# Optimization experiments

Measured on AMD Instinct MI355X. Metric: run time of the kernel, lower is better.

Reference implementation:

```python
import jax, jax.numpy as jnp
import numpy as np

D = 256; NH = 8; HD = 32; DFF = 1024; NL = 4; NPT = 4
SHAPES = [(100, 100), (50, 50), (25, 25), (13, 13)]
LEN_V = sum(h * w for h, w in SHAPES)  # 13294
BS = 16; LQ = 300


def _ln(x, g, b):
    m = jnp.mean(x, -1, keepdims=True)
    v = jnp.var(x, -1, keepdims=True)
    return (x - m) * jax.lax.rsqrt(v + 1e-5) * g + b


def _bilinear(v, loc, H, W):
    # v: [bs, nh, H*W, hd]; loc: [bs, Lq, nh, P, 2] normalized [0,1]
    # matches F.grid_sample(bilinear, align_corners=False, padding_mode='zeros')
    bs, Lq, nh, P, _ = loc.shape
    x = loc[..., 0] * W - 0.5
    y = loc[..., 1] * H - 0.5
    x0 = jnp.floor(x); y0 = jnp.floor(y)
    dx = x - x0; dy = y - y0
    x0 = x0.astype(jnp.int32); y0 = y0.astype(jnp.int32)
    out = jnp.zeros((bs, Lq, nh, P, v.shape[-1]), v.dtype)
    for ix, iy, w in ((x0, y0, (1 - dx) * (1 - dy)),
                      (x0 + 1, y0, dx * (1 - dy)),
                      (x0, y0 + 1, (1 - dx) * dy),
                      (x0 + 1, y0 + 1, dx * dy)):
        valid = (ix >= 0) & (ix < W) & (iy >= 0) & (iy < H)
        idx = jnp.clip(iy, 0, H - 1) * W + jnp.clip(ix, 0, W - 1)  # [bs,Lq,nh,P]
        idx = jnp.transpose(idx, (0, 2, 1, 3)).reshape(bs, nh, Lq * P, 1)
        g = jnp.take_along_axis(v, idx, axis=2).reshape(bs, nh, Lq, P, -1)
        g = jnp.transpose(g, (0, 2, 1, 3, 4))  # [bs,Lq,nh,P,hd]
        out = out + g * jnp.where(valid, w, jnp.zeros_like(w))[..., None]
    return out


def reference(tgt, reference_points, memory, Wq, bq, Wk, bk, Wv, bv, Wo, bo,
              Wvp, bvp, Wso, bso, Waw, baw, Wop, bop, W1, bf1, W2, bf2,
              ln1_g, ln1_b, ln2_g, ln2_b, ln3_g, ln3_b):
    bs, Lq, _ = tgt.shape
    # ---- self attention (query_pos_embed=None, attn_mask=None) ----
    qh = (tgt @ Wq + bq).reshape(bs, Lq, NH, HD)
    kh = (tgt @ Wk + bk).reshape(bs, Lq, NH, HD)
    vh = (tgt @ Wv + bv).reshape(bs, Lq, NH, HD)
    scores = jnp.einsum('bqhd,bkhd->bhqk', qh, kh) * np.float32(1.0 / np.sqrt(HD))
    attn = jax.nn.softmax(scores, -1)
    sa = jnp.einsum('bhqk,bkhd->bqhd', attn, vh).reshape(bs, Lq, D) @ Wo + bo
    t = _ln(tgt + sa, ln1_g, ln1_b)
    # ---- PP multi-scale deformable cross attention ----
    val = (memory @ Wvp + bvp).reshape(bs, LEN_V, NH, HD)
    val = jnp.transpose(val, (0, 2, 1, 3))  # [bs, nh, Lv, hd]
    off = (t @ Wso + bso).reshape(bs, Lq, NH, NL, NPT, 2)
    aw = jax.nn.softmax((t @ Waw + baw).reshape(bs, Lq, NH, NL * NPT), -1)
    aw = aw.reshape(bs, Lq, NH, NL, NPT)
    rp = reference_points  # [bs, Lq, NL, 4] -> (cx, cy, w, h) branch
    loc = rp[:, :, None, :, None, :2] + off / NPT * rp[:, :, None, :, None, 2:] * 0.5
    start = 0
    ca = jnp.zeros((bs, Lq, NH, HD), t.dtype)
    for l, (H, W) in enumerate(SHAPES):
        v_l = val[:, :, start:start + H * W]
        sampled = _bilinear(v_l, loc[:, :, :, l], H, W)  # [bs,Lq,nh,P,hd]
        ca = ca + jnp.einsum('bqhpd,bqhp->bqhd', sampled, aw[:, :, :, l])
        start += H * W
    ca = ca.reshape(bs, Lq, D) @ Wop + bop
    t = _ln(t + ca, ln2_g, ln2_b)
    # ---- FFN ----
    ff = jax.nn.relu(t @ W1 + bf1) @ W2 + bf2
    return _ln(t + ff, ln3_g, ln3_b)


def setup_inputs() -> dict:
    ks = iter(jax.random.split(jax.random.key(0), 64))
    inp = {}
    inp['tgt'] = jax.random.normal(next(ks), (BS, LQ, D), jnp.float32)
    inp['reference_points'] = jax.random.uniform(next(ks), (BS, LQ, NL, 4), jnp.float32)
    inp['memory'] = jax.random.normal(next(ks), (BS, LEN_V, D), jnp.float32)
    for name, sh in [('Wq', (D, D)), ('Wk', (D, D)), ('Wv', (D, D)), ('Wo', (D, D)),
                     ('Wvp', (D, D)), ('Wso', (D, NH * NL * NPT * 2)),
                     ('Waw', (D, NH * NL * NPT)), ('Wop', (D, D)),
                     ('W1', (D, DFF)), ('W2', (DFF, D))]:
        inp[name] = jax.random.normal(next(ks), sh, jnp.float32) * 0.02
    for name, dim in [('bq', D), ('bk', D), ('bv', D), ('bo', D), ('bvp', D),
                      ('bso', NH * NL * NPT * 2), ('baw', NH * NL * NPT),
                      ('bop', D), ('bf1', DFF), ('bf2', D)]:
        inp[name] = jnp.zeros((dim,), jnp.float32)
    for g, b in [('ln1_g', 'ln1_b'), ('ln2_g', 'ln2_b'), ('ln3_g', 'ln3_b')]:
        inp[g] = jnp.ones((D,), jnp.float32)
        inp[b] = jnp.zeros((D,), jnp.float32)
    return inp
```

## Files before the change

kernel.cpp:

```cpp
#include <hip/hip_runtime.h>
#include <hip/hip_bf16.h>
#include <cstddef>

#define D_    256
#define NH_   8
#define HD_   32
#define LQ_   300
#define BS_   16
#define LENV_ 13294
#define DFF_  1024
#define NROWS (BS_*LQ_)
#define VROWS (BS_*LENV_)

typedef __attribute__((ext_vector_type(8))) short short8;
typedef __attribute__((ext_vector_type(4))) float f32x4;
typedef unsigned int u32;

__device__ __forceinline__ short f2bf(float x) {
    unsigned u = __float_as_uint(x);
    u += 0x7fff + ((u >> 16) & 1);
    return (short)(u >> 16);
}
__device__ __forceinline__ unsigned pack_bf2(float lo, float hi) {
    return (unsigned)(unsigned short)f2bf(lo) | ((unsigned)(unsigned short)f2bf(hi) << 16);
}
__device__ __forceinline__ float bf2f(short s) {
    return __uint_as_float((unsigned)(unsigned short)s << 16);
}

__global__ __launch_bounds__(256) void prep_all(
    const float* __restrict__ Wq, const float* __restrict__ Wk,
    const float* __restrict__ Wv, const float* __restrict__ Wo,
    const float* __restrict__ Wvp, const float* __restrict__ Wso,
    const float* __restrict__ Waw, const float* __restrict__ Wop,
    const float* __restrict__ W1, const float* __restrict__ W2,
    const float* __restrict__ bqp, const float* __restrict__ bkp,
    const float* __restrict__ bvp, const float* __restrict__ bsop,
    const float* __restrict__ bawp,
    short* __restrict__ Wqkvt, short* __restrict__ Wot,
    short* __restrict__ Wvpt, short* __restrict__ Wsoawt,
    short* __restrict__ Wopt, short* __restrict__ W1t,
    short* __restrict__ W2t, float* __restrict__ bqkv,
    float* __restrict__ bsoaw)
{
    const int blk = blockIdx.x, tid = threadIdx.x;
    if (blk < 1792) {
        const int seg = blk >> 8;
        const int e = ((blk & 255) << 8) | tid;
        const int n = e >> 8, k = e & 255;
        const float* src; short* dst;
        switch (seg) {
            case 0: src = Wq;  dst = Wqkvt;          break;
            case 1: src = Wk;  dst = Wqkvt + 65536;  break;
            case 2: src = Wv;  dst = Wqkvt + 131072; break;
            case 3: src = Wo;  dst = Wot;            break;
            case 4: src = Wvp; dst = Wvpt;           break;
            case 5: src = Wso; dst = Wsoawt;         break;
            default: src = Wop; dst = Wopt;          break;
        }
        dst[e] = f2bf(src[(size_t)k * 256 + n]);
    } else if (blk < 1920) {
        const int e = ((blk - 1792) << 8) | tid;
        const int n = e >> 8, k = e & 255;
        Wsoawt[65536 + e] = f2bf(Waw[(size_t)k * 128 + n]);
    } else if (blk < 2048) {
        const int e = ((blk - 1920) << 8) | tid;
        Wsoawt[98304 + e] = 0;
    } else if (blk < 3072) {
        const int e = ((blk - 2048) << 8) | tid;
        const int n = e >> 8, k = e & 255;
        W1t[e] = f2bf(W1[(size_t)k * 1024 + n]);
    } else if (blk < 4096) {
        const int e = ((blk - 3072) << 8) | tid;
        const int n = e / 1024, k = e % 1024;
        W2t[e] = f2bf(W2[(size_t)k * 256 + n]);
    } else {
        const int e = ((blk - 4096) << 8) | tid;
        if (e < 768)
            bqkv[e] = (e < 256) ? bqp[e] : (e < 512) ? bkp[e - 256] : bvp[e - 512];
        else if (e < 1280) {
            const int f = e - 768;
            bsoaw[f] = (f < 256) ? bsop[f] : (f < 384) ? bawp[f - 256] : 0.f;
        }
    }
}

template<int ACT, int OUT_BF16, int STACKED, int FUSE_LN>
__global__ __launch_bounds__(256) void mfma_gemm(
    const float* __restrict__ A, const short* __restrict__ Wt,
    const float* __restrict__ bias, void* __restrict__ Cout,
    int M, int N, int K,
    const float* __restrict__ resid, const float* __restrict__ lng,
    const float* __restrict__ lnb)
{
    __shared__ short Alds[2][64 * 40];
    __shared__ short Blds[2][256 * 40];
    const int tid  = threadIdx.x;
    const int lane = tid & 63;
    const int wn   = tid >> 6;
    const int m0   = blockIdx.x * 64;
    const int nb   = blockIdx.y;
    const int srow = tid >> 2;
    const int schk = tid & 3;

    const int  arow = m0 + srow;
    const bool aok  = (arow < M);
    const float* aptr = &A[(size_t)(aok ? arow : 0) * K + schk * 8];
    const short* bptr = &Wt[(size_t)(nb * 256 + srow) * K + schk * 8];

    f32x4 acc[4][4] = {};
    float4 ra0, ra1;
    short8 rb0, rb1, rb2, rb3;

    ra0 = make_float4(0.f, 0.f, 0.f, 0.f); ra1 = ra0;
    if (aok) { ra0 = *(const float4*)(aptr); ra1 = *(const float4*)(aptr + 4); }
    rb0 = *(const short8*)(bptr);
    rb1 = *(const short8*)(bptr + (size_t)64 * K);
    rb2 = *(const short8*)(bptr + (size_t)128 * K);
    rb3 = *(const short8*)(bptr + (size_t)192 * K);
    {
        short8 s;
        s[0] = f2bf(ra0.x); s[1] = f2bf(ra0.y); s[2] = f2bf(ra0.z); s[3] = f2bf(ra0.w);
        s[4] = f2bf(ra1.x); s[5] = f2bf(ra1.y); s[6] = f2bf(ra1.z); s[7] = f2bf(ra1.w);
        *(short8*)&Alds[0][srow * 40 + schk * 8] = s;
        *(short8*)&Blds[0][(srow +   0) * 40 + schk * 8] = rb0;
        *(short8*)&Blds[0][(srow +  64) * 40 + schk * 8] = rb1;
        *(short8*)&Blds[0][(srow + 128) * 40 + schk * 8] = rb2;
        *(short8*)&Blds[0][(srow + 192) * 40 + schk * 8] = rb3;
    }
    __syncthreads();

    const int lg = lane >> 4;
    const int lr = lane & 15;
    int buf = 0;

    for (int k0 = 32; k0 < K; k0 += 32) {
        ra0 = make_float4(0.f, 0.f, 0.f, 0.f); ra1 = ra0;
        if (aok) { ra0 = *(const float4*)(aptr + k0); ra1 = *(const float4*)(aptr + k0 + 4); }
        rb0 = *(const short8*)(bptr + k0);
        rb1 = *(const short8*)(bptr + k0 + (size_t)64 * K);
        rb2 = *(const short8*)(bptr + k0 + (size_t)128 * K);
        rb3 = *(const short8*)(bptr + k0 + (size_t)192 * K);

        {
            short8 a[4], b[4];
            #pragma unroll
            for (int mr = 0; mr < 4; ++mr)
                a[mr] = *(const short8*)&Alds[buf][(mr * 16 + lr) * 40 + lg * 8];
            #pragma unroll
            for (int nr = 0; nr < 4; ++nr)
                b[nr] = *(const short8*)&Blds[buf][(wn * 64 + nr * 16 + lr) * 40 + lg * 8];
            #pragma unroll
            for (int mr = 0; mr < 4; ++mr)
                #pragma unroll
                for (int nr = 0; nr < 4; ++nr)
                    acc[mr][nr] = __builtin_amdgcn_mfma_f32_16x16x32_bf16(
                        a[mr], b[nr], acc[mr][nr], 0, 0, 0);
        }

        {
            short8 s;
            s[0] = f2bf(ra0.x); s[1] = f2bf(ra0.y); s[2] = f2bf(ra0.z); s[3] = f2bf(ra0.w);
            s[4] = f2bf(ra1.x); s[5] = f2bf(ra1.y); s[6] = f2bf(ra1.z); s[7] = f2bf(ra1.w);
            const int ob = buf ^ 1;
            *(short8*)&Alds[ob][srow * 40 + schk * 8] = s;
            *(short8*)&Blds[ob][(srow +   0) * 40 + schk * 8] = rb0;
            *(short8*)&Blds[ob][(srow +  64) * 40 + schk * 8] = rb1;
            *(short8*)&Blds[ob][(srow + 128) * 40 + schk * 8] = rb2;
            *(short8*)&Blds[ob][(srow + 192) * 40 + schk * 8] = rb3;
        }
        __syncthreads();
        buf ^= 1;
    }

    {
        short8 a[4], b[4];
        #pragma unroll
        for (int mr = 0; mr < 4; ++mr)
            a[mr] = *(const short8*)&Alds[buf][(mr * 16 + lr) * 40 + lg * 8];
        #pragma unroll
        for (int nr = 0; nr < 4; ++nr)
            b[nr] = *(const short8*)&Blds[buf][(wn * 64 + nr * 16 + lr) * 40 + lg * 8];
        #pragma unroll
        for (int mr = 0; mr < 4; ++mr)
            #pragma unroll
            for (int nr = 0; nr < 4; ++nr)
                acc[mr][nr] = __builtin_amdgcn_mfma_f32_16x16x32_bf16(
                    a[mr], b[nr], acc[mr][nr], 0, 0, 0);
    }

    if (FUSE_LN) {
        __shared__ float RedS[4][64];
        __shared__ float RedS2[4][64];
        float psum[4][4] = {};
        float psq[4][4]  = {};
        #pragma unroll
        for (int mr = 0; mr < 4; ++mr)
            #pragma unroll
            for (int r4 = 0; r4 < 4; ++r4) {
                const int row = m0 + mr * 16 + lg * 4 + r4;
                #pragma unroll
                for (int nr = 0; nr < 4; ++nr) {
                    const int col = wn * 64 + nr * 16 + lr;
                    float x = acc[mr][nr][r4] + bias[col]
                            + resid[(size_t)row * 256 + col];
                    acc[mr][nr][r4] = x;
                    psum[mr][r4] += x;
                    psq[mr][r4]  += x * x;
                }
            }
        #pragma unroll
        for (int o = 1; o < 16; o <<= 1)
            #pragma unroll
            for (int mr = 0; mr < 4; ++mr)
                #pragma unroll
                for (int r4 = 0; r4 < 4; ++r4) {
                    psum[mr][r4] += __shfl_xor(psum[mr][r4], o);
                    psq[mr][r4]  += __shfl_xor(psq[mr][r4], o);
                }
        if (lr == 0) {
            #pragma unroll
            for (int mr = 0; mr < 4; ++mr)
                #pragma unroll
                for (int r4 = 0; r4 < 4; ++r4) {
                    const int lrow = mr * 16 + lg * 4 + r4;
                    RedS[wn][lrow]  = psum[mr][r4];
                    RedS2[wn][lrow] = psq[mr][r4];
                }
        }
        __syncthreads();
        float* outp = (float*)Cout;
        #pragma unroll
        for (int mr = 0; mr < 4; ++mr)
            #pragma unroll
            for (int r4 = 0; r4 < 4; ++r4) {
                const int lrow = mr * 16 + lg * 4 + r4;
                const int row  = m0 + lrow;
                const float s  = RedS[0][lrow] + RedS[1][lrow] + RedS[2][lrow] + RedS[3][lrow];
                const float s2 = RedS2[0][lrow] + RedS2[1][lrow] + RedS2[2][lrow] + RedS2[3][lrow];
                const float mean = s * (1.f / 256.f);
                const float var  = s2 * (1.f / 256.f) - mean * mean;
                const float inv  = rsqrtf(var + 1e-5f);
                #pragma unroll
                for (int nr = 0; nr < 4; ++nr) {
                    const int col = wn * 64 + nr * 16 + lr;
                    outp[(size_t)row * 256 + col] =
                        (acc[mr][nr][r4] - mean) * inv * lng[col] + lnb[col];
                }
            }
        return;
    }

    if (STACKED) {
        float* Cb = (float*)Cout + (size_t)nb * M * 256;
        const float* bb = bias + nb * 256;
        #pragma unroll
        for (int mr = 0; mr < 4; ++mr)
            #pragma unroll
            for (int r = 0; r < 4; ++r) {
                const int row = m0 + mr * 16 + lg * 4 + r;
                if (row >= M) continue;
                #pragma unroll
                for (int nr = 0; nr < 4; ++nr) {
                    const int col = wn * 64 + nr * 16 + lr;
                    Cb[(size_t)row * 256 + col] = acc[mr][nr][r] + bb[col];
                }
            }
    } else {
        #pragma unroll
        for (int mr = 0; mr < 4; ++mr)
            #pragma unroll
            for (int r = 0; r < 4; ++r) {
                const int row = m0 + mr * 16 + lg * 4 + r;
                if (row >= M) continue;
                #pragma unroll
                for (int nr = 0; nr < 4; ++nr) {
                    const int col = nb * 256 + wn * 64 + nr * 16 + lr;
                    float v = acc[mr][nr][r] + bias[col];
                    if (ACT) v = fmaxf(v, 0.f);
                    if (OUT_BF16) ((short*)Cout)[(size_t)row * N + col] = f2bf(v);
                    else          ((float*)Cout)[(size_t)row * N + col] = v;
                }
            }
    }
}

__global__ __launch_bounds__(256, 2) void vp_gemm(
    const float* __restrict__ A, const short* __restrict__ Wt,
    const float* __restrict__ bias, short* __restrict__ C)
{
    __shared__ float Alds[2][32 * 256];
    __shared__ short Cst[32 * 256];
    const int tid  = threadIdx.x;
    const int lane = tid & 63;
    const int w    = tid >> 6;
    const int lr   = lane & 15;
    const int lg   = lane >> 4;

    short8 bf[4][8];
    #pragma unroll
    for (int nr = 0; nr < 4; ++nr) {
        const short* wp = &Wt[(size_t)(w * 64 + nr * 16 + lr) * 256 + lg * 8];
        #pragma unroll
        for (int kc = 0; kc < 8; ++kc)
            bf[nr][kc] = *(const short8*)(wp + kc * 32);
    }
    float bs[4];
    #pragma unroll
    for (int nr = 0; nr < 4; ++nr) bs[nr] = bias[w * 64 + nr * 16 + lr];

    const int NT = VROWS / 32;
    const int NB = 512;

    #define VP_STAGE(BUFI, TILE)                                               \
        {                                                                      \
            _Pragma("unroll")                                                  \
            for (int j = 0; j < 8; ++j) {                                      \
                const int r = w * 8 + j;                                       \
                const int grow = (TILE) * 32 + r;                              \
                const int c16 = ((((lane >> 1) ^ (r & 7)) << 1) | (lane & 1)); \
                const float* src = A + (size_t)grow * 256 + c16 * 4;           \
                __builtin_amdgcn_global_load_lds(                              \
                    (const __attribute__((address_space(1))) u32*)src,         \
                    (__attribute__((address_space(3))) u32*)&Alds[BUFI][r*256],\
                    16, 0, 0);                                                 \
            }                                                                  \
        }

    int t  = blockIdx.x;
    int t2 = t + NB;
    bool has2 = (t2 < NT);
    int buf = 0;

    VP_STAGE(0, t);
    if (has2) VP_STAGE(1, t2);
    if (has2) { asm volatile("s_waitcnt vmcnt(8)" ::: "memory"); }
    else      { asm volatile("s_waitcnt vmcnt(0)" ::: "memory"); }
    __builtin_amdgcn_sched_barrier(0);
    __builtin_amdgcn_s_barrier();

    while (true) {
        f32x4 acc[2][4] = {};
        #pragma unroll
        for (int kc = 0; kc < 8; ++kc) {
            short8 a[2];
            #pragma unroll
            for (int mr = 0; mr < 2; ++mr) {
                const int row = mr * 16 + lr;
                const int c32 = (kc * 4 + lg) ^ (row & 7);
                const float* p = &Alds[buf][row * 256 + c32 * 8];
                float4 x = *(const float4*)(p);
                float4 y = *(const float4*)(p + 4);
                short8 s;
                s[0] = f2bf(x.x); s[1] = f2bf(x.y); s[2] = f2bf(x.z); s[3] = f2bf(x.w);
                s[4] = f2bf(y.x); s[5] = f2bf(y.y); s[6] = f2bf(y.z); s[7] = f2bf(y.w);
                a[mr] = s;
            }
            #pragma unroll
            for (int mr = 0; mr < 2; ++mr)
                #pragma unroll
                for (int nr = 0; nr < 4; ++nr)
                    acc[mr][nr] = __builtin_amdgcn_mfma_f32_16x16x32_bf16(
                        a[mr], bf[nr][kc], acc[mr][nr], 0, 0, 0);
        }

        #pragma unroll
        for (int mr = 0; mr < 2; ++mr)
            #pragma unroll
            for (int r4 = 0; r4 < 4; ++r4)
                #pragma unroll
                for (int nr = 0; nr < 4; ++nr)
                    Cst[(mr * 16 + lg * 4 + r4) * 256 + w * 64 + nr * 16 + lr] =
                        f2bf(acc[mr][nr][r4] + bs[nr]);

        asm volatile("s_waitcnt lgkmcnt(0)" ::: "memory");
        __builtin_amdgcn_sched_barrier(0);
        __builtin_amdgcn_s_barrier();

        const int t3 = t2 + NB;
        const bool has3 = has2 && (t3 < NT);
        if (has3) VP_STAGE(buf, t3);

        {
            const size_t base = (size_t)t * 32 * 256;
            #pragma unroll
            for (int j = 0; j < 4; ++j) {
                const int chunk = j * 256 + tid;
                *(short8*)&C[base + (size_t)chunk * 8] =
                    *(const short8*)&Cst[chunk * 8];
            }
        }

        if (has2) {
            if (has3) { asm volatile("s_waitcnt vmcnt(12)" ::: "memory"); }
            else      { asm volatile("s_waitcnt vmcnt(4)"  ::: "memory"); }
        }
        __builtin_amdgcn_sched_barrier(0);
        __builtin_amdgcn_s_barrier();

        if (!has2) break;
        buf ^= 1;
        t = t2; t2 = t3; has2 = has3;
    }
    #undef VP_STAGE
}

__global__ __launch_bounds__(256) void attn_fused(
    const float* __restrict__ qh, const float* __restrict__ kh,
    const float* __restrict__ vh, float* __restrict__ sa)
{
    __shared__ short Klds[304 * 40];
    __shared__ short Vtlds[32 * 328];
    const int bh = blockIdx.x, b = bh / NH_, h = bh % NH_;
    const int tid = threadIdx.x;

    for (int idx = tid; idx < 304 * 4; idx += 256) {
        const int key = idx >> 2, dc = idx & 3;
        short8 s = {};
        if (key < LQ_) {
            const float* kp = &kh[((size_t)(b * LQ_ + key)) * D_ + h * HD_ + dc * 8];
            float4 a0 = *reinterpret_cast<const float4*>(kp);
            float4 a1 = *reinterpret_cast<const float4*>(kp + 4);
            s[0] = f2bf(a0.x); s[1] = f2bf(a0.y); s[2] = f2bf(a0.z); s[3] = f2bf(a0.w);
            s[4] = f2bf(a1.x); s[5] = f2bf(a1.y); s[6] = f2bf(a1.z); s[7] = f2bf(a1.w);
        }
        *reinterpret_cast<short8*>(&Klds[key * 40 + dc * 8]) = s;
    }
    for (int idx = tid; idx < LQ_ * 8; idx += 256) {
        const int key = idx >> 3, dc = idx & 7;
        const float4 v4 = *reinterpret_cast<const float4*>(
            &vh[((size_t)(b * LQ_ + key)) * D_ + h * HD_ + dc * 4]);
        Vtlds[(dc * 4 + 0) * 328 + key] = f2bf(v4.x);
        Vtlds[(dc * 4 + 1) * 328 + key] = f2bf(v4.y);
        Vtlds[(dc * 4 + 2) * 328 + key] = f2bf(v4.z);
        Vtlds[(dc * 4 + 3) * 328 + key] = f2bf(v4.w);
    }
    for (int idx = tid; idx < 32 * 20; idx += 256) {
        const int d = idx / 20, kk = idx % 20;
        Vtlds[d * 328 + 300 + kk] = 0;
    }
    __syncthreads();

    const int lane = tid & 63;
    const int wid  = tid >> 6;
    const int g    = lane >> 4;
    const int qc   = lane & 15;
    const int y    = blockIdx.y;
    const int qt_end = (y == 0) ? 10 : 19;

    for (int qt = y * 10 + wid; qt < qt_end; qt += 4) {
        const int q0 = qt * 16;
        short8 qf;
        {
            const int q = min(q0 + qc, LQ_ - 1);
            const float* qp = &qh[((size_t)(b * LQ_ + q)) * D_ + h * HD_ + g * 8];
            float4 a0 = *reinterpret_cast<const float4*>(qp);
            float4 a1 = *reinterpret_cast<const float4*>(qp + 4);
            const float sc = 0.17677669529663687f;
            qf[0] = f2bf(a0.x * sc); qf[1] = f2bf(a0.y * sc);
            qf[2] = f2bf(a0.z * sc); qf[3] = f2bf(a0.w * sc);
            qf[4] = f2bf(a1.x * sc); qf[5] = f2bf(a1.y * sc);
            qf[6] = f2bf(a1.z * sc); qf[7] = f2bf(a1.w * sc);
        }
        f32x4 s[19];
        #pragma unroll
        for (int kt = 0; kt < 19; ++kt) {
            short8 kf = *reinterpret_cast<const short8*>(&Klds[(kt * 16 + qc) * 40 + g * 8]);
            f32x4 z = {};
            s[kt] = __builtin_amdgcn_mfma_f32_16x16x32_bf16(kf, qf, z, 0, 0, 0);
        }
        if (g == 3) { s[18][0] = -1e30f; s[18][1] = -1e30f; s[18][2] = -1e30f; s[18][3] = -1e30f; }

        float m = -1e30f;
        #pragma unroll
        for (int kt = 0; kt < 19; ++kt)
            #pragma unroll
            for (int r = 0; r < 4; ++r) m = fmaxf(m, s[kt][r]);
        m = fmaxf(m, __shfl_xor(m, 16));
        m = fmaxf(m, __shfl_xor(m, 32));
        float sum = 0.f;
        #pragma unroll
        for (int kt = 0; kt < 19; ++kt)
            #pragma unroll
            for (int r = 0; r < 4; ++r) {
                float e = __expf(s[kt][r] - m);
                s[kt][r] = e; sum += e;
            }
        sum += __shfl_xor(sum, 16);
        sum += __shfl_xor(sum, 32);
        const float inv = 1.f / sum;

        unsigned pb0[20], pb1[20];
        #pragma unroll
        for (int kt = 0; kt < 19; ++kt) {
            pb0[kt] = pack_bf2(s[kt][0] * inv, s[kt][1] * inv);
            pb1[kt] = pack_bf2(s[kt][2] * inv, s[kt][3] * inv);
        }
        pb0[19] = 0; pb1[19] = 0;

        f32x4 acc0 = {}, acc1 = {};
        const int src0 = ((g & 1) << 5) + qc;
        const int src1 = src0 + 16;
        const bool hi = (g >> 1);
        #pragma unroll
        for (int c = 0; c < 10; ++c) {
            short8 va0 = *reinterpret_cast<const short8*>(&Vtlds[qc * 328 + c * 32 + g * 8]);
            short8 va1 = *reinterpret_cast<const short8*>(&Vtlds[(qc + 16) * 328 + c * 32 + g * 8]);
            int x0a = __shfl((int)pb0[2 * c], src0), x0b = __shfl((int)pb0[2 * c + 1], src0);
            int x1a = __shfl((int)pb1[2 * c], src0), x1b = __shfl((int)pb1[2 * c + 1], src0);
            int x2a = __shfl((int)pb0[2 * c], src1), x2b = __shfl((int)pb0[2 * c + 1], src1);
            int x3a = __shfl((int)pb1[2 * c], src1), x3b = __shfl((int)pb1[2 * c + 1], src1);
            union { int u[4]; short8 s8; } pb;
            pb.u[0] = hi ? x0b : x0a;
            pb.u[1] = hi ? x1b : x1a;
            pb.u[2] = hi ? x2b : x2a;
            pb.u[3] = hi ? x3b : x3a;
            acc0 = __builtin_amdgcn_mfma_f32_16x16x32_bf16(va0, pb.s8, acc0, 0, 0, 0);
            acc1 = __builtin_amdgcn_mfma_f32_16x16x32_bf16(va1, pb.s8, acc1, 0, 0, 0);
        }

        if (q0 + qc < LQ_) {
            float* op = &sa[((size_t)(b * LQ_ + q0 + qc)) * D_ + h * HD_ + 4 * g];
            *reinterpret_cast<float4*>(op)      = make_float4(acc0[0], acc0[1], acc0[2], acc0[3]);
            *reinterpret_cast<float4*>(op + 16) = make_float4(acc1[0], acc1[1], acc1[2], acc1[3]);
        }
    }
}

__global__ __launch_bounds__(256) void deform_kernel(
    const __hip_bfloat16* __restrict__ val, const float* __restrict__ off,
    const float* __restrict__ aw, const float* __restrict__ rp,
    float* __restrict__ ca)
{
    const int i = blockIdx.x * 256 + threadIdx.x;
    if (i >= NROWS * NH_ * 4) return;
    const int dq = i & 3;
    const int h  = (i >> 2) & 7;
    const int bq = i >> 5;
    const int b  = bq / LQ_;

    const int Hs[4] = {100, 50, 25, 13};
    const int st[4] = {0, 10000, 12500, 13125};

    const float* rpp  = rp  + (size_t)bq * 16;
    const float* offp = off + (size_t)bq * 256 + h * 32;
    const float* awp  = aw  + (size_t)bq * 256 + h * 16;
    const short* vb   = (const short*)val + ((size_t)b * LENV_) * D_ + h * HD_ + dq * 8;

    float wv[16], wmax = -1e30f, wsum = 0.f;
    #pragma unroll
    for (int j = 0; j < 16; ++j) { wv[j] = awp[j]; wmax = fmaxf(wmax, wv[j]); }
    #pragma unroll
    for (int j = 0; j < 16; ++j) { wv[j] = __expf(wv[j] - wmax); wsum += wv[j]; }
    const float winv = 1.f / wsum;

    float acc[8] = {};
    #pragma unroll
    for (int l = 0; l < 4; ++l) {
        const float cx = rpp[l * 4 + 0], cy = rpp[l * 4 + 1];
        const float sw = rpp[l * 4 + 2], sh = rpp[l * 4 + 3];
        const int H = Hs[l], W = Hs[l];
        const int base = st[l];
        #pragma unroll
        for (int p = 0; p < 4; ++p) {
            const float ox = offp[l * 8 + p * 2 + 0];
            const float oy = offp[l * 8 + p * 2 + 1];
            const float x = (cx + ox * 0.125f * sw) * W - 0.5f;
            const float y = (cy + oy * 0.125f * sh) * H - 0.5f;
            const float x0f = floorf(x), y0f = floorf(y);
            const float dx = x - x0f, dy = y - y0f;
            const int x0 = (int)x0f, y0 = (int)y0f;
            const float a = wv[l * 4 + p] * winv;

            float tp[8] = {};
            #pragma unroll
            for (int t = 0; t < 4; ++t) {
                const int ix = x0 + (t & 1);
                const int iy = y0 + (t >> 1);
                const float wx = (t & 1) ? dx : (1.f - dx);
                const float wy = (t >> 1) ? dy : (1.f - dy);
                const bool valid = (ix >= 0) & (ix < W) & (iy >= 0) & (iy < H);
                const int cxi = min(max(ix, 0), W - 1);
                const int cyi = min(max(iy, 0), H - 1);
                const float w = valid ? wx * wy : 0.f;
                const short8 u = *reinterpret_cast<const short8*>(
                    &vb[(size_t)(base + cyi * W + cxi) * D_]);
                #pragma unroll
                for (int k = 0; k < 8; ++k)
                    tp[k] = fmaf(w, bf2f(u[k]), tp[k]);
            }
            #pragma unroll
            for (int k = 0; k < 8; ++k)
                acc[k] = fmaf(a, tp[k], acc[k]);
        }
    }
    float* op = &ca[(size_t)i * 8];
    *reinterpret_cast<float4*>(op)     = make_float4(acc[0], acc[1], acc[2], acc[3]);
    *reinterpret_cast<float4*>(op + 4) = make_float4(acc[4], acc[5], acc[6], acc[7]);
}

extern "C" void kernel_launch(void* const* d_in, const int* in_sizes, int n_in,
                              void* d_out, int out_size, void* d_ws, size_t ws_size,
                              hipStream_t stream)
{
    const float* tgt    = (const float*)d_in[0];
    const float* refpts = (const float*)d_in[1];
    const float* memory = (const float*)d_in[2];
    const float* Wq  = (const float*)d_in[3];
    const float* Wk  = (const float*)d_in[4];
    const float* Wv  = (const float*)d_in[5];
    const float* Wo  = (const float*)d_in[6];
    const float* Wvp = (const float*)d_in[7];
    const float* Wso = (const float*)d_in[8];
    const float* Waw = (const float*)d_in[9];
    const float* Wop = (const float*)d_in[10];
    const float* W1  = (const float*)d_in[11];
    const float* W2  = (const float*)d_in[12];
    const float* bq  = (const float*)d_in[13];
    const float* bk  = (const float*)d_in[14];
    const float* bv  = (const float*)d_in[15];
    const float* bo  = (const float*)d_in[16];
    const float* bvp = (const float*)d_in[17];
    const float* bso = (const float*)d_in[18];
    const float* baw = (const float*)d_in[19];
    const float* bop = (const float*)d_in[20];
    const float* bf1 = (const float*)d_in[21];
    const float* bf2 = (const float*)d_in[22];
    const float* ln1g = (const float*)d_in[23];
    const float* ln1b = (const float*)d_in[24];
    const float* ln2g = (const float*)d_in[25];
    const float* ln2b = (const float*)d_in[26];
    const float* ln3g = (const float*)d_in[27];
    const float* ln3b = (const float*)d_in[28];
    float* out = (float*)d_out;

    const size_t SZ = (size_t)NROWS * D_;
    float* ws = (float*)d_ws;
    float* reg1 = ws;
    float* reg2 = ws + SZ;
    float* reg3 = ws + 2 * SZ;
    float* t    = ws + 3 * SZ;
    float* t2   = ws + 4 * SZ;
    float* big  = ws + 5 * SZ;

    float* qh = reg1;
    float* kh = reg2;
    float* vh = reg3;
    float* sa_heads = t2;
    __hip_bfloat16* val = (__hip_bfloat16*)big;
    float* off_raw = reg2;
    float* aw_raw  = reg3;
    float* ca_heads = reg1;
    float* ff1 = big;

    char* wtbase = (char*)d_ws + 5 * SZ * sizeof(float) + (size_t)VROWS * D_ * 2;
    short* Wqkvt  = (short*)wtbase;
    short* Wot    = Wqkvt  + 196608;
    short* Wvpt   = Wot    + 65536;
    short* Wsoawt = Wvpt   + 65536;
    short* Wopt   = Wsoawt + 131072;
    short* W1t    = Wopt   + 65536;
    short* W2t    = W1t    + 262144;
    float* bqkv   = (float*)(W2t + 262144);
    float* bsoaw  = bqkv + 768;

    const dim3 blk(256);

    prep_all<<<dim3(4101), blk, 0, stream>>>(
        Wq, Wk, Wv, Wo, Wvp, Wso, Waw, Wop, W1, W2,
        bq, bk, bv, bso, baw,
        Wqkvt, Wot, Wvpt, Wsoawt, Wopt, W1t, W2t, bqkv, bsoaw);

    mfma_gemm<0,0,1,0><<<dim3(75, 3), blk, 0, stream>>>(
        tgt, Wqkvt, bqkv, reg1, NROWS, 256, D_, nullptr, nullptr, nullptr);

    attn_fused<<<dim3(BS_ * NH_, 2), blk, 0, stream>>>(qh, kh, vh, sa_heads);

    mfma_gemm<0,0,0,1><<<dim3(75, 1), blk, 0, stream>>>(
        sa_heads, Wot, bo, t, NROWS, 256, D_, tgt, ln1g, ln1b);

    vp_gemm<<<dim3(512), blk, 0, stream>>>(memory, Wvpt, bvp, (short*)val);

    mfma_gemm<0,0,1,0><<<dim3(75, 2), blk, 0, stream>>>(
        t, Wsoawt, bsoaw, reg2, NROWS, 256, D_, nullptr, nullptr, nullptr);

    deform_kernel<<<dim3((NROWS * NH_ * 4 + 255) / 256), blk, 0, stream>>>(
        val, off_raw, aw_raw, refpts, ca_heads);

    mfma_gemm<0,0,0,1><<<dim3(75, 1), blk, 0, stream>>>(
        ca_heads, Wopt, bop, t2, NROWS, 256, D_, t, ln2g, ln2b);

    mfma_gemm<1,0,0,0><<<dim3(75, 4), blk, 0, stream>>>(
        t2, W1t, bf1, ff1, NROWS, DFF_, D_, nullptr, nullptr, nullptr);
    mfma_gemm<0,0,0,1><<<dim3(75, 1), blk, 0, stream>>>(
        ff1, W2t, bf2, out, NROWS, 256, DFF_, t2, ln3g, ln3b);
}
```

Before: 223.6 us.

## Restructure value-projection GEMM: weights in LDS, per-wave tiles with register prefetch

After: 681.1 us. 3.05x slower.

```diff
diff --git a/kernel.cpp b/kernel.cpp
--- a/kernel.cpp
+++ b/kernel.cpp
@@ -11,8 +11,10 @@
 #define DFF_  1024
 #define NROWS (BS_*LQ_)
 #define VROWS (BS_*LENV_)
+#define NTILE 13294
 
 typedef __attribute__((ext_vector_type(8))) short short8;
+typedef __attribute__((ext_vector_type(4))) short short4v;
 typedef __attribute__((ext_vector_type(4))) float f32x4;
 typedef unsigned int u32;
 
@@ -285,124 +287,90 @@
     }
 }
 
-__global__ __launch_bounds__(256, 2) void vp_gemm(
+__global__ __launch_bounds__(512, 2) void vp_gemm(
     const float* __restrict__ A, const short* __restrict__ Wt,
     const float* __restrict__ bias, short* __restrict__ C)
 {
-    __shared__ float Alds[2][32 * 256];
-    __shared__ short Cst[32 * 256];
+    __shared__ short Blds[65536];
+    __shared__ float bias_lds[256];
     const int tid  = threadIdx.x;
     const int lane = tid & 63;
-    const int w    = tid >> 6;
+    const int wv   = tid >> 6;
     const int lr   = lane & 15;
     const int lg   = lane >> 4;
 
-    short8 bf[4][8];
-    #pragma unroll
-    for (int nr = 0; nr < 4; ++nr) {
-        const short* wp = &Wt[(size_t)(w * 64 + nr * 16 + lr) * 256 + lg * 8];
-        #pragma unroll
-        for (int kc = 0; kc < 8; ++kc)
-            bf[nr][kc] = *(const short8*)(wp + kc * 32);
-    }
-    float bs[4];
-    #pragma unroll
-    for (int nr = 0; nr < 4; ++nr) bs[nr] = bias[w * 64 + nr * 16 + lr];
-
-    const int NT = VROWS / 32;
-    const int NB = 512;
-
-    #define VP_STAGE(BUFI, TILE)                                               \
-        {                                                                      \
-            _Pragma("unroll")                                                  \
-            for (int j = 0; j < 8; ++j) {                                      \
-                const int r = w * 8 + j;                                       \
-                const int grow = (TILE) * 32 + r;                              \
-                const int c16 = ((((lane >> 1) ^ (r & 7)) << 1) | (lane & 1)); \
-                const float* src = A + (size_t)grow * 256 + c16 * 4;           \
-                __builtin_amdgcn_global_load_lds(                              \
-                    (const __attribute__((address_space(1))) u32*)src,         \
-                    (__attribute__((address_space(3))) u32*)&Alds[BUFI][r*256],\
-                    16, 0, 0);                                                 \
-            }                                                                  \
-        }
-
-    int t  = blockIdx.x;
-    int t2 = t + NB;
-    bool has2 = (t2 < NT);
-    int buf = 0;
-
-    VP_STAGE(0, t);
-    if (has2) VP_STAGE(1, t2);
-    if (has2) { asm volatile("s_waitcnt vmcnt(8)" ::: "memory"); }
-    else      { asm volatile("s_waitcnt vmcnt(0)" ::: "memory"); }
-    __builtin_amdgcn_sched_barrier(0);
-    __builtin_amdgcn_s_barrier();
+    for (int c = tid; c < 8192; c += 512) {
+        const int lgs = c & 3;
+        const int col = (c >> 2) & 255;
+        const int kc  = c >> 10;
+        short8 v = *(const short8*)&Wt[(size_t)col * 256 + kc * 32 + lgs * 8];
+        *(short8*)&Blds[c * 8] = v;
+    }
+    if (tid < 256) bias_lds[tid] = bias[tid];
+    __syncthreads();
+
+    const int NW = 2048;
+    const int wid = blockIdx.x * 8 + wv;
+
+    #define VP_LOAD(dst, T)                                                  \
+        {                                                                    \
+            const float* ap = A + ((size_t)(T) * 16 + lr) * 256 + lg * 8;    \
+            _Pragma("unroll")                                                \
+            for (int kc = 0; kc < 8; ++kc) {                                 \
+                dst[2 * kc]     = *(const float4*)(ap + kc * 32);            \
+                dst[2 * kc + 1] = *(const float4*)(ap + kc * 32 + 4);        \
+            }                                                                \
+        }
+
+    #define VP_BODY(src, T)                                                  \
+        {                                                                    \
+            f32x4 acc[16] = {};                                              \
+            _Pragma("unroll")                                                \
+            for (int kc = 0; kc < 8; ++kc) {                                 \
+                const float4 x = src[2 * kc], y = src[2 * kc + 1];           \
+                short8 af;                                                   \
+                af[0] = f2bf(x.x); af[1] = f2bf(x.y);                        \
+                af[2] = f2bf(x.z); af[3] = f2bf(x.w);                        \
+                af[4] = f2bf(y.x); af[5] = f2bf(y.y);                        \
+                af[6] = f2bf(y.z); af[7] = f2bf(y.w);                        \
+                _Pragma("unroll")                                            \
+                for (int nr = 0; nr < 16; ++nr) {                            \
+                    short8 bf8 = *(const short8*)&Blds[                      \
+                        ((((kc << 8) + (nr << 4) + lr) << 2) + lg) * 8];     \
+                    acc[nr] = __builtin_amdgcn_mfma_f32_16x16x32_bf16(       \
+                        bf8, af, acc[nr], 0, 0, 0);                          \
+                }                                                            \
+            }                                                                \
+            const int tnext = (T) + 2 * NW;                                  \
+            if (tnext < NTILE) VP_LOAD(src, tnext);                          \
+            short* cp = C + ((size_t)(T) * 16 + lr) * 256;                   \
+            _Pragma("unroll")                                                \
+            for (int nr = 0; nr < 16; ++nr) {                                \
+                float4 bs = *(const float4*)&bias_lds[nr * 16 + lg * 4];     \
+                short4v s4;                                                  \
+                s4[0] = f2bf(acc[nr][0] + bs.x);                             \
+                s4[1] = f2bf(acc[nr][1] + bs.y);                             \
+                s4[2] = f2bf(acc[nr][2] + bs.z);                             \
+                s4[3] = f2bf(acc[nr][3] + bs.w);                             \
+                *(short4v*)&cp[nr * 16 + lg * 4] = s4;                       \
+            }                                                                \
+        }
+
+    float4 pA[16], pB[16];
+    int ta = wid;
+    int tb = wid + NW;
+    VP_LOAD(pA, ta);
+    if (tb < NTILE) VP_LOAD(pB, tb);
 
     while (true) {
-        f32x4 acc[2][4] = {};
-        #pragma unroll
-        for (int kc = 0; kc < 8; ++kc) {
-            short8 a[2];
-            #pragma unroll
-            for (int mr = 0; mr < 2; ++mr) {
-                const int row = mr * 16 + lr;
-                const int c32 = (kc * 4 + lg) ^ (row & 7);
-                const float* p = &Alds[buf][row * 256 + c32 * 8];
-                float4 x = *(const float4*)(p);
-                float4 y = *(const float4*)(p + 4);
-                short8 s;
-                s[0] = f2bf(x.x); s[1] = f2bf(x.y); s[2] = f2bf(x.z); s[3] = f2bf(x.w);
-                s[4] = f2bf(y.x); s[5] = f2bf(y.y); s[6] = f2bf(y.z); s[7] = f2bf(y.w);
-                a[mr] = s;
-            }
-            #pragma unroll
-            for (int mr = 0; mr < 2; ++mr)
-                #pragma unroll
-                for (int nr = 0; nr < 4; ++nr)
-                    acc[mr][nr] = __builtin_amdgcn_mfma_f32_16x16x32_bf16(
-                        a[mr], bf[nr][kc], acc[mr][nr], 0, 0, 0);
-        }
-
-        #pragma unroll
-        for (int mr = 0; mr < 2; ++mr)
-            #pragma unroll
-            for (int r4 = 0; r4 < 4; ++r4)
-                #pragma unroll
-                for (int nr = 0; nr < 4; ++nr)
-                    Cst[(mr * 16 + lg * 4 + r4) * 256 + w * 64 + nr * 16 + lr] =
-                        f2bf(acc[mr][nr][r4] + bs[nr]);
-
-        asm volatile("s_waitcnt lgkmcnt(0)" ::: "memory");
-        __builtin_amdgcn_sched_barrier(0);
-        __builtin_amdgcn_s_barrier();
-
-        const int t3 = t2 + NB;
-        const bool has3 = has2 && (t3 < NT);
-        if (has3) VP_STAGE(buf, t3);
-
-        {
-            const size_t base = (size_t)t * 32 * 256;
-            #pragma unroll
-            for (int j = 0; j < 4; ++j) {
-                const int chunk = j * 256 + tid;
-                *(short8*)&C[base + (size_t)chunk * 8] =
-                    *(const short8*)&Cst[chunk * 8];
-            }
-        }
-
-        if (has2) {
-            if (has3) { asm volatile("s_waitcnt vmcnt(12)" ::: "memory"); }
-            else      { asm volatile("s_waitcnt vmcnt(4)"  ::: "memory"); }
-        }
-        __builtin_amdgcn_sched_barrier(0);
-        __builtin_amdgcn_s_barrier();
-
-        if (!has2) break;
-        buf ^= 1;
-        t = t2; t2 = t3; has2 = has3;
-    }
-    #undef VP_STAGE
+        VP_BODY(pA, ta);
+        if (tb >= NTILE) break;
+        VP_BODY(pB, tb);
+        ta += 2 * NW; tb += 2 * NW;
+        if (ta >= NTILE) break;
+    }
+    #undef VP_LOAD
+    #undef VP_BODY
 }
 
 __global__ __launch_bounds__(256) void attn_fused(
@@ -679,7 +647,7 @@
     mfma_gemm<0,0,0,1><<<dim3(75, 1), blk, 0, stream>>>(
         sa_heads, Wot, bo, t, NROWS, 256, D_, tgt, ln1g, ln1b);
 
-    vp_gemm<<<dim3(512), blk, 0, stream>>>(memory, Wvpt, bvp, (short*)val);
+    vp_gemm<<<dim3(256), dim3(512), 0, stream>>>(memory, Wvpt, bvp, (short*)val);
 
     mfma_gemm<0,0,1,0><<<dim3(75, 2), blk, 0, stream>>>(
         t, Wsoawt, bsoaw, reg2, NROWS, 256, D_, nullptr, nullptr, nullptr);
```
